# Optimization experiments

Measured on AMD Instinct MI355X. Metric: run time of the kernel, lower is better.

Reference implementation:

```python
import jax, jax.numpy as jnp
import numpy as np

NUM_HEADS = 8
NUM_POINTS = 4


def setup_inputs() -> dict:
    key = jax.random.key(0)
    bs, h, w = 2, 128, 128
    cin = cout = 256
    nq = h * w
    ks = jax.random.split(key, 6)
    query = jax.random.normal(ks[0], (bs, nq, cin), jnp.float32)
    value = jax.random.normal(ks[1], (bs, nq, cin), jnp.float32)
    # sampling_offsets: small random weight, bias = directional grid init (as in init_weights)
    W_off = jax.random.normal(ks[2], (cin, NUM_HEADS * NUM_POINTS * 2), jnp.float32) * 0.01
    thetas = np.arange(NUM_HEADS, dtype=np.float32) * (2.0 * np.pi / NUM_HEADS)
    grid = np.stack([np.cos(thetas), np.sin(thetas)], -1)
    grid = grid / np.abs(grid).max(-1, keepdims=True)
    grid = np.tile(grid[:, None, :], (1, NUM_POINTS, 1)) * (np.arange(NUM_POINTS, dtype=np.float32)[None, :, None] + 1.0)
    b_off = jnp.asarray(grid.reshape(-1), jnp.float32)
    W_attn = jax.random.normal(ks[3], (cin, NUM_HEADS * NUM_POINTS), jnp.float32) * 0.01
    b_attn = jnp.zeros((NUM_HEADS * NUM_POINTS,), jnp.float32)
    s = 1.0 / np.sqrt(cin)  # xavier-ish uniform
    W_val = jax.random.uniform(ks[4], (cin, cout), jnp.float32, -s, s)
    b_val = jnp.zeros((cout,), jnp.float32)
    W_out = jax.random.uniform(ks[5], (cout, cout), jnp.float32, -s, s)
    b_out = jnp.zeros((cout,), jnp.float32)
    return {"query": query, "value": value, "W_off": W_off, "b_off": b_off,
            "W_attn": W_attn, "b_attn": b_attn, "W_val": W_val, "b_val": b_val,
            "W_out": W_out, "b_out": b_out, "h": h, "w": w}


def _bilinear_sample(v_flat, ix, iy, h, w):
    # v_flat: (bs, heads, h*w, d); ix/iy: (bs, heads, nq, P) pixel coords.
    # grid_sample bilinear, align_corners=False, padding_mode='zeros'.
    x0 = jnp.floor(ix)
    y0 = jnp.floor(iy)
    wx1 = ix - x0
    wy1 = iy - y0
    bs, hd, nq, P = ix.shape
    acc = 0.0
    corners = ((x0, y0, (1.0 - wx1) * (1.0 - wy1)),
               (x0 + 1.0, y0, wx1 * (1.0 - wy1)),
               (x0, y0 + 1.0, (1.0 - wx1) * wy1),
               (x0 + 1.0, y0 + 1.0, wx1 * wy1))
    for xc, yc, wgt in corners:
        xi = xc.astype(jnp.int32)
        yi = yc.astype(jnp.int32)
        valid = (xi >= 0) & (xi < w) & (yi >= 0) & (yi < h)
        idx = jnp.clip(yi, 0, h - 1) * w + jnp.clip(xi, 0, w - 1)
        g = jnp.take_along_axis(v_flat, idx.reshape(bs, hd, nq * P)[..., None], axis=2)
        acc = acc + g.reshape(bs, hd, nq, P, -1) * (wgt * valid)[..., None]
    return acc  # (bs, heads, nq, P, d)


def deform_attn(query, value, W_off, b_off, W_attn, b_attn, W_val, b_val, h, w):
    bs, nq, _ = query.shape
    d = W_val.shape[1] // NUM_HEADS
    v = (value @ W_val + b_val).reshape(bs, nq, NUM_HEADS, d)
    off = (query @ W_off + b_off).reshape(bs, nq, NUM_HEADS, NUM_POINTS, 2)
    aw = jax.nn.softmax((query @ W_attn + b_attn).reshape(bs, nq, NUM_HEADS, NUM_POINTS), axis=-1)
    # reference points in [0,1], scale_ratio=1.0, (x, y) order
    ys = (jnp.arange(h, dtype=jnp.float32) + 0.5) / h
    xs = (jnp.arange(w, dtype=jnp.float32) + 0.5) / w
    ry, rx = jnp.meshgrid(ys, xs, indexing='ij')
    ref = jnp.stack([rx.reshape(-1), ry.reshape(-1)], -1)  # (nq, 2)
    loc = ref[None, :, None, None, :] + off / jnp.array([w, h], jnp.float32)
    grid = 2.0 * loc - 1.0  # normalized grid_sample coords
    grid = grid.transpose(0, 2, 1, 3, 4)  # (bs, heads, nq, P, 2)
    ix = (grid[..., 0] + 1.0) * (w / 2.0) - 0.5
    iy = (grid[..., 1] + 1.0) * (h / 2.0) - 0.5
    v_flat = v.transpose(0, 2, 1, 3)  # (bs, heads, h*w, d)
    sampled = _bilinear_sample(v_flat, ix, iy, h, w)  # (bs, heads, nq, P, d)
    out = (sampled * aw.transpose(0, 2, 1, 3)[..., None]).sum(3)  # (bs, heads, nq, d)
    return out.transpose(0, 2, 1, 3).reshape(bs, nq, NUM_HEADS * d)


def reference(query, value, W_off, b_off, W_attn, b_attn, W_val, b_val, W_out, b_out, h, w):
    attn = deform_attn(query, value, W_off, b_off, W_attn, b_attn, W_val, b_val, h, w)
    # dropout acts as identity in eval mode; identity residual = query
    return attn @ W_out + b_out + query
```

## Files before the change

### kernel.cpp

```cpp
#include <hip/hip_runtime.h>
#include <type_traits>

#define H_IMG 128
#define W_IMG 128
#define NQ (H_IMG * W_IMG)
#define CIN 256
#define NH 8
#define NP 4
#define DH 32

typedef __bf16 bf16x4 __attribute__((ext_vector_type(4)));
typedef __bf16 bf16x8 __attribute__((ext_vector_type(8)));
typedef float f32x4 __attribute__((ext_vector_type(4)));

__global__ __launch_bounds__(256) void prep_weights(
    const float* __restrict__ Wval, const float* __restrict__ Wout,
    const float* __restrict__ Woff, const float* __restrict__ Wattn,
    const float* __restrict__ boff, const float* __restrict__ battn,
    __bf16* __restrict__ btv, __bf16* __restrict__ bto,
    __bf16* __restrict__ btoa, float* __restrict__ bias96) {
  int id = blockIdx.x * 256 + threadIdx.x;
  if (id < 256 * 256) {
    int n = id >> 8, k = id & 255;
    btv[n * 256 + k] = (__bf16)Wval[k * 256 + n];
    bto[n * 256 + k] = (__bf16)Wout[k * 256 + n];
  }
  if (id < 96 * 256) {
    int n = id >> 8, k = id & 255;
    float w = (n < 64) ? Woff[k * 64 + n] : Wattn[k * 32 + (n - 64)];
    btoa[n * 256 + k] = (__bf16)w;
  }
  if (id < 96) {
    bias96[id] = (id < 64) ? boff[id] : battn[id - 64];
  }
}

template <typename TA, typename TC, bool PLANAR, bool ADD>
__global__ __launch_bounds__(256) void gemm128(
    const TA* __restrict__ A, const __bf16* __restrict__ BT,
    const float* __restrict__ bias, const float* __restrict__ addm,
    TC* __restrict__ C, int M) {
  const int t = threadIdx.x;
  const int lane = t & 63;
  const int wave = t >> 6;
  const int r = lane & 15;
  const int q = lane >> 4;
  const int gm0 = blockIdx.x * 128;
  const int gn0 = blockIdx.y * 64;
  const int wm = (wave & 1) * 64;
  const int wn = (wave >> 1) * 32;

  __shared__ __bf16 As[128 * 40];
  __shared__ __bf16 Bs[64 * 40];

  f32x4 acc[4][2];
#pragma unroll
  for (int mt = 0; mt < 4; ++mt)
#pragma unroll
    for (int nt = 0; nt < 2; ++nt) acc[mt][nt] = (f32x4){0.f, 0.f, 0.f, 0.f};

  for (int kt = 0; kt < 8; ++kt) {
    const int k0 = kt * 32;
    __syncthreads();
    if constexpr (std::is_same<TA, float>::value) {
#pragma unroll
      for (int it = 0; it < 2; ++it) {
        int row = it * 64 + (t >> 2);
        int kc = (t & 3) * 8;
        const float* src = A + (size_t)(gm0 + row) * 256 + k0 + kc;
        float4 f0 = *(const float4*)src;
        float4 f1 = *(const float4*)(src + 4);
        bf16x8 hh;
        hh[0] = (__bf16)f0.x; hh[1] = (__bf16)f0.y;
        hh[2] = (__bf16)f0.z; hh[3] = (__bf16)f0.w;
        hh[4] = (__bf16)f1.x; hh[5] = (__bf16)f1.y;
        hh[6] = (__bf16)f1.z; hh[7] = (__bf16)f1.w;
        *(bf16x8*)(&As[row * 40 + kc]) = hh;
      }
    } else {
#pragma unroll
      for (int it = 0; it < 2; ++it) {
        int row = it * 64 + (t >> 2);
        int kc = (t & 3) * 8;
        *(bf16x8*)(&As[row * 40 + kc]) =
            *(const bf16x8*)(A + (size_t)(gm0 + row) * 256 + k0 + kc);
      }
    }
    {
      int row = t >> 2;
      int kc = (t & 3) * 8;
      *(bf16x8*)(&Bs[row * 40 + kc]) =
          *(const bf16x8*)(BT + (size_t)(gn0 + row) * 256 + k0 + kc);
    }
    __syncthreads();
    bf16x8 bfr[2];
#pragma unroll
    for (int nt = 0; nt < 2; ++nt)
      bfr[nt] = *(const bf16x8*)(&Bs[(wn + nt * 16 + r) * 40 + q * 8]);
#pragma unroll
    for (int mt = 0; mt < 4; ++mt) {
      bf16x8 a = *(const bf16x8*)(&As[(wm + mt * 16 + r) * 40 + q * 8]);
#pragma unroll
      for (int nt = 0; nt < 2; ++nt)
        acc[mt][nt] =
            __builtin_amdgcn_mfma_f32_16x16x32_bf16(a, bfr[nt], acc[mt][nt], 0, 0, 0);
    }
  }

#pragma unroll
  for (int mt = 0; mt < 4; ++mt)
#pragma unroll
    for (int nt = 0; nt < 2; ++nt)
#pragma unroll
      for (int rr = 0; rr < 4; ++rr) {
        int row = gm0 + wm + mt * 16 + q * 4 + rr;
        int col = gn0 + wn + nt * 16 + r;
        float val = acc[mt][nt][rr] + bias[col];
        if constexpr (ADD) val += addm[(size_t)row * 256 + col];
        if constexpr (PLANAR)
          C[((size_t)(col >> 5) * M + row) * 32 + (col & 31)] = (TC)val;
        else
          C[(size_t)row * 256 + col] = (TC)val;
      }
}

#define AS_STRIDE 40
__global__ __launch_bounds__(256) void gemm_oa(
    const float* __restrict__ A, const __bf16* __restrict__ BT,
    const float* __restrict__ bias, float* __restrict__ C) {
  const int t = threadIdx.x;
  const int lane = t & 63;
  const int wave = t >> 6;
  const int r = lane & 15;
  const int q = lane >> 4;
  const int gm0 = blockIdx.x * 64;
  const int n0 = (wave >> 1) * 48;
  const int mw = (wave & 1) * 32;
  const int NTW = 3;

  __shared__ __bf16 As[64 * AS_STRIDE];

  f32x4 acc[2][3];
#pragma unroll
  for (int mt = 0; mt < 2; ++mt)
#pragma unroll
    for (int nt = 0; nt < NTW; ++nt) acc[mt][nt] = (f32x4){0.f, 0.f, 0.f, 0.f};

  for (int kt = 0; kt < 8; ++kt) {
    const int k0 = kt * 32;
    __syncthreads();
#pragma unroll
    for (int it = 0; it < 2; ++it) {
      int row = it * 32 + (t >> 3);
      int kc = (t & 7) * 4;
      float4 f = *(const float4*)(A + (size_t)(gm0 + row) * 256 + k0 + kc);
      bf16x4 hh;
      hh[0] = (__bf16)f.x; hh[1] = (__bf16)f.y;
      hh[2] = (__bf16)f.z; hh[3] = (__bf16)f.w;
      *(bf16x4*)(&As[row * AS_STRIDE + kc]) = hh;
    }
    __syncthreads();
    bf16x8 bfr[NTW];
#pragma unroll
    for (int nt = 0; nt < NTW; ++nt)
      bfr[nt] = *(const bf16x8*)(BT + (size_t)(n0 + nt * 16 + r) * 256 + k0 + q * 8);
#pragma unroll
    for (int mt = 0; mt < 2; ++mt) {
      bf16x8 a = *(const bf16x8*)(&As[(mw + mt * 16 + r) * AS_STRIDE + q * 8]);
#pragma unroll
      for (int nt = 0; nt < NTW; ++nt)
        acc[mt][nt] =
            __builtin_amdgcn_mfma_f32_16x16x32_bf16(a, bfr[nt], acc[mt][nt], 0, 0, 0);
    }
  }

#pragma unroll
  for (int mt = 0; mt < 2; ++mt)
#pragma unroll
    for (int nt = 0; nt < NTW; ++nt)
#pragma unroll
      for (int rr = 0; rr < 4; ++rr) {
        int row = gm0 + mw + mt * 16 + q * 4 + rr;
        int col = n0 + nt * 16 + r;
        C[(size_t)row * 96 + col] = acc[mt][nt][rr] + bias[col];
      }
}

__global__ __launch_bounds__(256) void sample_kernel(
    const __bf16* __restrict__ v, const float* __restrict__ oa,
    __bf16* __restrict__ attn, int M) {
  const int lane = threadIdx.x & 63;
  const int wave = threadIdx.x >> 6;
  const int ql = lane >> 5;
  const int head = (lane >> 2) & 7;
  const int c8 = (lane & 3) * 8;
  const int QPW = 8;
  int base_row = (blockIdx.x * 4 + wave) * QPW + ql;
  const __bf16* vh = v + (size_t)head * M * 32 + c8;
  for (int it = 0; it < QPW; it += 2) {
    int row = base_row + it;
    int b = row >> 14;
    int qi = row & (NQ - 1);
    int x = qi & (W_IMG - 1);
    int y = qi >> 7;
    const float* oarow = oa + (size_t)row * 96;
    float l0 = oarow[64 + head * 4 + 0];
    float l1 = oarow[64 + head * 4 + 1];
    float l2 = oarow[64 + head * 4 + 2];
    float l3 = oarow[64 + head * 4 + 3];
    float mx = fmaxf(fmaxf(l0, l1), fmaxf(l2, l3));
    float e0 = __expf(l0 - mx), e1 = __expf(l1 - mx);
    float e2 = __expf(l2 - mx), e3 = __expf(l3 - mx);
    float inv = 1.f / (e0 + e1 + e2 + e3);
    float awp[4] = {e0 * inv, e1 * inv, e2 * inv, e3 * inv};
    float acc[8] = {0.f, 0.f, 0.f, 0.f, 0.f, 0.f, 0.f, 0.f};
    const __bf16* vb = vh + (size_t)b * NQ * 32;
#pragma unroll
    for (int p = 0; p < NP; ++p) {
      float ox = oarow[head * 8 + p * 2 + 0];
      float oy = oarow[head * 8 + p * 2 + 1];
      float ix = (float)x + ox;
      float iy = (float)y + oy;
      float x0f = floorf(ix), y0f = floorf(iy);
      float wx1 = ix - x0f, wy1 = iy - y0f;
      int x0 = (int)x0f, y0 = (int)y0f;
      float wgt[4] = {(1.f - wx1) * (1.f - wy1), wx1 * (1.f - wy1),
                      (1.f - wx1) * wy1, wx1 * wy1};
      int xs[4] = {x0, x0 + 1, x0, x0 + 1};
      int ysv[4] = {y0, y0, y0 + 1, y0 + 1};
#pragma unroll
      for (int c = 0; c < 4; ++c) {
        int xi = xs[c], yi = ysv[c];
        bool valid = (xi >= 0) & (xi < W_IMG) & (yi >= 0) & (yi < H_IMG);
        int xc = xi < 0 ? 0 : (xi > W_IMG - 1 ? W_IMG - 1 : xi);
        int yc = yi < 0 ? 0 : (yi > H_IMG - 1 ? H_IMG - 1 : yi);
        float wv = awp[p] * wgt[c] * (valid ? 1.f : 0.f);
        bf16x8 g = *(const bf16x8*)(vb + (size_t)(yc * W_IMG + xc) * 32);
#pragma unroll
        for (int j = 0; j < 8; ++j) acc[j] += wv * (float)g[j];
      }
    }
    bf16x8 o;
#pragma unroll
    for (int j = 0; j < 8; ++j) o[j] = (__bf16)acc[j];
    *(bf16x8*)(attn + (size_t)row * 256 + head * DH + c8) = o;
  }
}

extern "C" void kernel_launch(void* const* d_in, const int* in_sizes, int n_in,
                              void* d_out, int out_size, void* d_ws, size_t ws_size,
                              hipStream_t stream) {
  const float* query  = (const float*)d_in[0];
  const float* value  = (const float*)d_in[1];
  const float* W_off  = (const float*)d_in[2];
  const float* b_off  = (const float*)d_in[3];
  const float* W_attn = (const float*)d_in[4];
  const float* b_attn = (const float*)d_in[5];
  const float* W_val  = (const float*)d_in[6];
  const float* b_val  = (const float*)d_in[7];
  const float* W_out  = (const float*)d_in[8];
  const float* b_out  = (const float*)d_in[9];
  float* out = (float*)d_out;

  char* ws = (char*)d_ws;
  __bf16* btv    = (__bf16*)(ws + 0);
  __bf16* bto    = (__bf16*)(ws + 131072);
  __bf16* btoa   = (__bf16*)(ws + 262144);
  float*  bias96 = (float*)(ws + 311296);
  __bf16* v      = (__bf16*)(ws + 524288);
  float*  oa     = (float*)(ws + 17301504);
  __bf16* attn   = (__bf16*)(ws + 29884416);

  const int M = in_sizes[0] / CIN;

  prep_weights<<<256, 256, 0, stream>>>(W_val, W_out, W_off, W_attn,
                                        b_off, b_attn, btv, bto, btoa, bias96);
  gemm128<float, __bf16, true, false><<<dim3(M / 128, 4), 256, 0, stream>>>(
      value, btv, b_val, nullptr, v, M);
  gemm_oa<<<M / 64, 256, 0, stream>>>(query, btoa, bias96, oa);
  sample_kernel<<<M / 32, 256, 0, stream>>>(v, oa, attn, M);
  gemm128<__bf16, float, false, true><<<dim3(M / 128, 4), 256, 0, stream>>>(
      attn, bto, b_out, query, out, M);
}
```

Before: 185.9 us.

## Fuse offset/attention GEMM into sampling kernel and restage GEMMs with full-K LDS tiles

Merges the query projection for offsets and attention logits into the bilinear sampling kernel. The 96-column result now stays in shared memory instead of going through a global buffer, which removes one kernel launch and a global round-trip of the oa tensor. The value and output GEMMs are restructured to 64x64 tiles that load the whole K=256 slab into LDS once, with a padded stride, removing the per-k-step barriers. The trade-off is higher LDS use per block, which may limit occupancy. The sampling loop now has each thread walk all 8 heads serially for one query, which changes the gather access pattern.

```diff
diff --git a/kernel.cpp b/kernel.cpp
--- a/kernel.cpp
+++ b/kernel.cpp
@@ -8,6 +8,7 @@
 #define NH 8
 #define NP 4
 #define DH 32
+#define LDSP 264
 
 typedef __bf16 bf16x4 __attribute__((ext_vector_type(4)));
 typedef __bf16 bf16x8 __attribute__((ext_vector_type(8)));
@@ -36,7 +37,7 @@
 }
 
 template <typename TA, typename TC, bool PLANAR, bool ADD>
-__global__ __launch_bounds__(256) void gemm128(
+__global__ __launch_bounds__(256) void gemm64(
     const TA* __restrict__ A, const __bf16* __restrict__ BT,
     const float* __restrict__ bias, const float* __restrict__ addm,
     TC* __restrict__ C, int M) {
@@ -45,70 +46,64 @@
   const int wave = t >> 6;
   const int r = lane & 15;
   const int q = lane >> 4;
-  const int gm0 = blockIdx.x * 128;
+  const int gm0 = blockIdx.x * 64;
   const int gn0 = blockIdx.y * 64;
-  const int wm = (wave & 1) * 64;
+  const int wm = (wave & 1) * 32;
   const int wn = (wave >> 1) * 32;
 
-  __shared__ __bf16 As[128 * 40];
-  __shared__ __bf16 Bs[64 * 40];
-
-  f32x4 acc[4][2];
-#pragma unroll
-  for (int mt = 0; mt < 4; ++mt)
+  __shared__ __bf16 As[64 * LDSP];
+  __shared__ __bf16 Bs[64 * LDSP];
+
+  if constexpr (std::is_same<TA, float>::value) {
+#pragma unroll
+    for (int i = 0; i < 16; ++i) {
+      int g = i * 256 + t;
+      int row = g >> 6, c4 = g & 63;
+      float4 f = *(const float4*)(A + (size_t)(gm0 + row) * 256 + c4 * 4);
+      bf16x4 hh;
+      hh[0] = (__bf16)f.x; hh[1] = (__bf16)f.y;
+      hh[2] = (__bf16)f.z; hh[3] = (__bf16)f.w;
+      *(bf16x4*)(&As[row * LDSP + c4 * 4]) = hh;
+    }
+  } else {
+#pragma unroll
+    for (int i = 0; i < 8; ++i) {
+      int g = i * 256 + t;
+      int row = g >> 5, c = g & 31;
+      *(bf16x8*)(&As[row * LDSP + c * 8]) =
+          *(const bf16x8*)(A + (size_t)(gm0 + row) * 256 + c * 8);
+    }
+  }
+#pragma unroll
+  for (int i = 0; i < 8; ++i) {
+    int g = i * 256 + t;
+    int row = g >> 5, c = g & 31;
+    *(bf16x8*)(&Bs[row * LDSP + c * 8]) =
+        *(const bf16x8*)(BT + (size_t)(gn0 + row) * 256 + c * 8);
+  }
+  __syncthreads();
+
+  f32x4 acc[2][2];
+#pragma unroll
+  for (int mt = 0; mt < 2; ++mt)
 #pragma unroll
     for (int nt = 0; nt < 2; ++nt) acc[mt][nt] = (f32x4){0.f, 0.f, 0.f, 0.f};
 
+#pragma unroll
   for (int kt = 0; kt < 8; ++kt) {
-    const int k0 = kt * 32;
-    __syncthreads();
-    if constexpr (std::is_same<TA, float>::value) {
-#pragma unroll
-      for (int it = 0; it < 2; ++it) {
-        int row = it * 64 + (t >> 2);
-        int kc = (t & 3) * 8;
-        const float* src = A + (size_t)(gm0 + row) * 256 + k0 + kc;
-        float4 f0 = *(const float4*)src;
-        float4 f1 = *(const float4*)(src + 4);
-        bf16x8 hh;
-        hh[0] = (__bf16)f0.x; hh[1] = (__bf16)f0.y;
-        hh[2] = (__bf16)f0.z; hh[3] = (__bf16)f0.w;
-        hh[4] = (__bf16)f1.x; hh[5] = (__bf16)f1.y;
-        hh[6] = (__bf16)f1.z; hh[7] = (__bf16)f1.w;
-        *(bf16x8*)(&As[row * 40 + kc]) = hh;
-      }
-    } else {
-#pragma unroll
-      for (int it = 0; it < 2; ++it) {
-        int row = it * 64 + (t >> 2);
-        int kc = (t & 3) * 8;
-        *(bf16x8*)(&As[row * 40 + kc]) =
-            *(const bf16x8*)(A + (size_t)(gm0 + row) * 256 + k0 + kc);
-      }
-    }
-    {
-      int row = t >> 2;
-      int kc = (t & 3) * 8;
-      *(bf16x8*)(&Bs[row * 40 + kc]) =
-          *(const bf16x8*)(BT + (size_t)(gn0 + row) * 256 + k0 + kc);
-    }
-    __syncthreads();
-    bf16x8 bfr[2];
-#pragma unroll
-    for (int nt = 0; nt < 2; ++nt)
-      bfr[nt] = *(const bf16x8*)(&Bs[(wn + nt * 16 + r) * 40 + q * 8]);
-#pragma unroll
-    for (int mt = 0; mt < 4; ++mt) {
-      bf16x8 a = *(const bf16x8*)(&As[(wm + mt * 16 + r) * 40 + q * 8]);
-#pragma unroll
-      for (int nt = 0; nt < 2; ++nt)
-        acc[mt][nt] =
-            __builtin_amdgcn_mfma_f32_16x16x32_bf16(a, bfr[nt], acc[mt][nt], 0, 0, 0);
-    }
-  }
-
-#pragma unroll
-  for (int mt = 0; mt < 4; ++mt)
+    const int ko = kt * 32 + q * 8;
+    bf16x8 a0 = *(const bf16x8*)(&As[(wm + r) * LDSP + ko]);
+    bf16x8 a1 = *(const bf16x8*)(&As[(wm + 16 + r) * LDSP + ko]);
+    bf16x8 b0 = *(const bf16x8*)(&Bs[(wn + r) * LDSP + ko]);
+    bf16x8 b1 = *(const bf16x8*)(&Bs[(wn + 16 + r) * LDSP + ko]);
+    acc[0][0] = __builtin_amdgcn_mfma_f32_16x16x32_bf16(a0, b0, acc[0][0], 0, 0, 0);
+    acc[0][1] = __builtin_amdgcn_mfma_f32_16x16x32_bf16(a0, b1, acc[0][1], 0, 0, 0);
+    acc[1][0] = __builtin_amdgcn_mfma_f32_16x16x32_bf16(a1, b0, acc[1][0], 0, 0, 0);
+    acc[1][1] = __builtin_amdgcn_mfma_f32_16x16x32_bf16(a1, b1, acc[1][1], 0, 0, 0);
+  }
+
+#pragma unroll
+  for (int mt = 0; mt < 2; ++mt)
 #pragma unroll
     for (int nt = 0; nt < 2; ++nt)
 #pragma unroll
@@ -124,101 +119,92 @@
       }
 }
 
-#define AS_STRIDE 40
-__global__ __launch_bounds__(256) void gemm_oa(
-    const float* __restrict__ A, const __bf16* __restrict__ BT,
-    const float* __restrict__ bias, float* __restrict__ C) {
+__global__ __launch_bounds__(256) void oa_sample(
+    const float* __restrict__ query, const __bf16* __restrict__ btoa,
+    const float* __restrict__ bias96, const __bf16* __restrict__ v,
+    __bf16* __restrict__ attn, int M) {
   const int t = threadIdx.x;
   const int lane = t & 63;
   const int wave = t >> 6;
   const int r = lane & 15;
   const int q = lane >> 4;
   const int gm0 = blockIdx.x * 64;
+  const int wm = (wave & 1) * 32;
   const int n0 = (wave >> 1) * 48;
-  const int mw = (wave & 1) * 32;
-  const int NTW = 3;
-
-  __shared__ __bf16 As[64 * AS_STRIDE];
+
+  __shared__ __bf16 As[64 * LDSP];
+  __shared__ float oas[64 * 100];
+
+#pragma unroll
+  for (int i = 0; i < 16; ++i) {
+    int g = i * 256 + t;
+    int row = g >> 6, c4 = g & 63;
+    float4 f = *(const float4*)(query + (size_t)(gm0 + row) * 256 + c4 * 4);
+    bf16x4 hh;
+    hh[0] = (__bf16)f.x; hh[1] = (__bf16)f.y;
+    hh[2] = (__bf16)f.z; hh[3] = (__bf16)f.w;
+    *(bf16x4*)(&As[row * LDSP + c4 * 4]) = hh;
+  }
+  __syncthreads();
 
   f32x4 acc[2][3];
 #pragma unroll
   for (int mt = 0; mt < 2; ++mt)
 #pragma unroll
-    for (int nt = 0; nt < NTW; ++nt) acc[mt][nt] = (f32x4){0.f, 0.f, 0.f, 0.f};
-
+    for (int nt = 0; nt < 3; ++nt) acc[mt][nt] = (f32x4){0.f, 0.f, 0.f, 0.f};
+
+#pragma unroll
   for (int kt = 0; kt < 8; ++kt) {
-    const int k0 = kt * 32;
-    __syncthreads();
-#pragma unroll
-    for (int it = 0; it < 2; ++it) {
-      int row = it * 32 + (t >> 3);
-      int kc = (t & 7) * 4;
-      float4 f = *(const float4*)(A + (size_t)(gm0 + row) * 256 + k0 + kc);
-      bf16x4 hh;
-      hh[0] = (__bf16)f.x; hh[1] = (__bf16)f.y;
-      hh[2] = (__bf16)f.z; hh[3] = (__bf16)f.w;
-      *(bf16x4*)(&As[row * AS_STRIDE + kc]) = hh;
-    }
-    __syncthreads();
-    bf16x8 bfr[NTW];
-#pragma unroll
-    for (int nt = 0; nt < NTW; ++nt)
-      bfr[nt] = *(const bf16x8*)(BT + (size_t)(n0 + nt * 16 + r) * 256 + k0 + q * 8);
-#pragma unroll
-    for (int mt = 0; mt < 2; ++mt) {
-      bf16x8 a = *(const bf16x8*)(&As[(mw + mt * 16 + r) * AS_STRIDE + q * 8]);
-#pragma unroll
-      for (int nt = 0; nt < NTW; ++nt)
-        acc[mt][nt] =
-            __builtin_amdgcn_mfma_f32_16x16x32_bf16(a, bfr[nt], acc[mt][nt], 0, 0, 0);
-    }
-  }
-
-#pragma unroll
-  for (int mt = 0; mt < 2; ++mt)
-#pragma unroll
-    for (int nt = 0; nt < NTW; ++nt)
+    const int ko = kt * 32 + q * 8;
+    bf16x8 a0 = *(const bf16x8*)(&As[(wm + r) * LDSP + ko]);
+    bf16x8 a1 = *(const bf16x8*)(&As[(wm + 16 + r) * LDSP + ko]);
+    bf16x8 b[3];
+#pragma unroll
+    for (int nt = 0; nt < 3; ++nt)
+      b[nt] = *(const bf16x8*)(btoa + (size_t)(n0 + nt * 16 + r) * 256 + ko);
+#pragma unroll
+    for (int nt = 0; nt < 3; ++nt) {
+      acc[0][nt] = __builtin_amdgcn_mfma_f32_16x16x32_bf16(a0, b[nt], acc[0][nt], 0, 0, 0);
+      acc[1][nt] = __builtin_amdgcn_mfma_f32_16x16x32_bf16(a1, b[nt], acc[1][nt], 0, 0, 0);
+    }
+  }
+#pragma unroll
+  for (int mt = 0; mt < 2; ++mt)
+#pragma unroll
+    for (int nt = 0; nt < 3; ++nt)
 #pragma unroll
       for (int rr = 0; rr < 4; ++rr) {
-        int row = gm0 + mw + mt * 16 + q * 4 + rr;
+        int rl = wm + mt * 16 + q * 4 + rr;
         int col = n0 + nt * 16 + r;
-        C[(size_t)row * 96 + col] = acc[mt][nt][rr] + bias[col];
+        oas[rl * 100 + col] = acc[mt][nt][rr] + bias96[col];
       }
-}
-
-__global__ __launch_bounds__(256) void sample_kernel(
-    const __bf16* __restrict__ v, const float* __restrict__ oa,
-    __bf16* __restrict__ attn, int M) {
-  const int lane = threadIdx.x & 63;
-  const int wave = threadIdx.x >> 6;
-  const int ql = lane >> 5;
-  const int head = (lane >> 2) & 7;
-  const int c8 = (lane & 3) * 8;
-  const int QPW = 8;
-  int base_row = (blockIdx.x * 4 + wave) * QPW + ql;
-  const __bf16* vh = v + (size_t)head * M * 32 + c8;
-  for (int it = 0; it < QPW; it += 2) {
-    int row = base_row + it;
-    int b = row >> 14;
-    int qi = row & (NQ - 1);
-    int x = qi & (W_IMG - 1);
-    int y = qi >> 7;
-    const float* oarow = oa + (size_t)row * 96;
-    float l0 = oarow[64 + head * 4 + 0];
-    float l1 = oarow[64 + head * 4 + 1];
-    float l2 = oarow[64 + head * 4 + 2];
-    float l3 = oarow[64 + head * 4 + 3];
+  __syncthreads();
+
+  const int qrow = t >> 2;
+  const int c8 = (t & 3) * 8;
+  const int row = gm0 + qrow;
+  const int b = row >> 14;
+  const int qi = row & (NQ - 1);
+  const int x = qi & (W_IMG - 1);
+  const int y = qi >> 7;
+  const float* oar = &oas[qrow * 100];
+#pragma unroll
+  for (int h = 0; h < NH; ++h) {
+    float l0 = oar[64 + h * 4 + 0];
+    float l1 = oar[64 + h * 4 + 1];
+    float l2 = oar[64 + h * 4 + 2];
+    float l3 = oar[64 + h * 4 + 3];
     float mx = fmaxf(fmaxf(l0, l1), fmaxf(l2, l3));
     float e0 = __expf(l0 - mx), e1 = __expf(l1 - mx);
     float e2 = __expf(l2 - mx), e3 = __expf(l3 - mx);
     float inv = 1.f / (e0 + e1 + e2 + e3);
     float awp[4] = {e0 * inv, e1 * inv, e2 * inv, e3 * inv};
-    float acc[8] = {0.f, 0.f, 0.f, 0.f, 0.f, 0.f, 0.f, 0.f};
-    const __bf16* vb = vh + (size_t)b * NQ * 32;
+    float fa[8] = {0.f, 0.f, 0.f, 0.f, 0.f, 0.f, 0.f, 0.f};
+    const __bf16* vh = v + ((size_t)h * M + (size_t)b * NQ) * 32 + c8;
 #pragma unroll
     for (int p = 0; p < NP; ++p) {
-      float ox = oarow[head * 8 + p * 2 + 0];
-      float oy = oarow[head * 8 + p * 2 + 1];
+      float ox = oar[h * 8 + p * 2 + 0];
+      float oy = oar[h * 8 + p * 2 + 1];
       float ix = (float)x + ox;
       float iy = (float)y + oy;
       float x0f = floorf(ix), y0f = floorf(iy);
@@ -235,15 +221,15 @@
         int xc = xi < 0 ? 0 : (xi > W_IMG - 1 ? W_IMG - 1 : xi);
         int yc = yi < 0 ? 0 : (yi > H_IMG - 1 ? H_IMG - 1 : yi);
         float wv = awp[p] * wgt[c] * (valid ? 1.f : 0.f);
-        bf16x8 g = *(const bf16x8*)(vb + (size_t)(yc * W_IMG + xc) * 32);
-#pragma unroll
-        for (int j = 0; j < 8; ++j) acc[j] += wv * (float)g[j];
+        bf16x8 g = *(const bf16x8*)(vh + (size_t)(yc * W_IMG + xc) * 32);
+#pragma unroll
+        for (int j = 0; j < 8; ++j) fa[j] += wv * (float)g[j];
       }
     }
     bf16x8 o;
 #pragma unroll
-    for (int j = 0; j < 8; ++j) o[j] = (__bf16)acc[j];
-    *(bf16x8*)(attn + (size_t)row * 256 + head * DH + c8) = o;
+    for (int j = 0; j < 8; ++j) o[j] = (__bf16)fa[j];
+    *(bf16x8*)(attn + (size_t)row * 256 + h * DH + c8) = o;
   }
 }
 
@@ -268,17 +254,15 @@
   __bf16* btoa   = (__bf16*)(ws + 262144);
   float*  bias96 = (float*)(ws + 311296);
   __bf16* v      = (__bf16*)(ws + 524288);
-  float*  oa     = (float*)(ws + 17301504);
-  __bf16* attn   = (__bf16*)(ws + 29884416);
+  __bf16* attn   = (__bf16*)(ws + 17301504);
 
   const int M = in_sizes[0] / CIN;
 
   prep_weights<<<256, 256, 0, stream>>>(W_val, W_out, W_off, W_attn,
                                         b_off, b_attn, btv, bto, btoa, bias96);
-  gemm128<float, __bf16, true, false><<<dim3(M / 128, 4), 256, 0, stream>>>(
+  gemm64<float, __bf16, true, false><<<dim3(M / 64, 4), 256, 0, stream>>>(
       value, btv, b_val, nullptr, v, M);
-  gemm_oa<<<M / 64, 256, 0, stream>>>(query, btoa, bias96, oa);
-  sample_kernel<<<M / 32, 256, 0, stream>>>(v, oa, attn, M);
-  gemm128<__bf16, float, false, true><<<dim3(M / 128, 4), 256, 0, stream>>>(
+  oa_sample<<<M / 64, 256, 0, stream>>>(query, btoa, bias96, v, attn, M);
+  gemm64<__bf16, float, false, true><<<dim3(M / 64, 4), 256, 0, stream>>>(
       attn, bto, b_out, query, out, M);
 }
```

New measurement: 175.0 us. -5.9%, faster.
